# Optimization experiments

Hardware: AMD Instinct MI355X
Metric: run time of the kernel (lower is better)

Reference implementation:

```python
import jax, jax.numpy as jnp
import numpy as np

N = 100000
IN_C = 128
OUT_C = 32
HEADS = 4
E = 1600000
NEG_SLOPE = 0.2


def setup_inputs() -> dict:
    key = jax.random.key(0)
    ks = jax.random.split(key, 8)
    x = jax.random.normal(ks[0], (N, IN_C), dtype=jnp.float32)
    edge_index = jax.random.randint(ks[1], (2, E), 0, N, dtype=jnp.int64)
    # GATConv params (PyG conventions): lin weight [H*C, in], att vectors [H, C], bias [H*C]
    sc = 1.0 / np.sqrt(IN_C)
    W = jax.random.uniform(ks[2], (HEADS * OUT_C, IN_C), dtype=jnp.float32, minval=-sc, maxval=sc)
    att_src = jax.random.normal(ks[3], (HEADS, OUT_C), dtype=jnp.float32) * 0.1
    att_dst = jax.random.normal(ks[4], (HEADS, OUT_C), dtype=jnp.float32) * 0.1
    bias_conv = jnp.zeros((HEADS * OUT_C,), dtype=jnp.float32)
    # final nn.Linear(H*C, C)
    sl = 1.0 / np.sqrt(HEADS * OUT_C)
    W_lin = jax.random.uniform(ks[5], (OUT_C, HEADS * OUT_C), dtype=jnp.float32, minval=-sl, maxval=sl)
    b_lin = jax.random.uniform(ks[6], (OUT_C,), dtype=jnp.float32, minval=-sl, maxval=sl)
    return {"x": x, "edge_index": edge_index, "W": W, "att_src": att_src,
            "att_dst": att_dst, "bias_conv": bias_conv, "W_lin": W_lin, "b_lin": b_lin}


def reference(x, edge_index, W, att_src, att_dst, bias_conv, W_lin, b_lin):
    n = x.shape[0]
    # add self loops (PyG default)
    loops = jnp.arange(n, dtype=edge_index.dtype)
    src = jnp.concatenate([edge_index[0], loops])
    dst = jnp.concatenate([edge_index[1], loops])
    # linear projection, per-head split: [N, H, C]
    h = (x @ W.T).reshape(n, HEADS, OUT_C)
    # per-node attention logits
    a_src = jnp.einsum('nhc,hc->nh', h, att_src)  # [N, H]
    a_dst = jnp.einsum('nhc,hc->nh', h, att_dst)  # [N, H]
    e = a_src[src] + a_dst[dst]                   # [E', H]
    e = jax.nn.leaky_relu(e, NEG_SLOPE)
    # segment softmax over incoming edges per destination node
    m = jax.ops.segment_max(e, dst, num_segments=n)       # [N, H]
    e = jnp.exp(e - m[dst])
    s = jax.ops.segment_sum(e, dst, num_segments=n)       # [N, H]
    alpha = e / s[dst]                                    # [E', H]
    # scatter-aggregate alpha-weighted source features
    msg = alpha[:, :, None] * h[src]                      # [E', H, C]
    out = jax.ops.segment_sum(msg, dst, num_segments=n)   # [N, H, C]
    out = out.reshape(n, HEADS * OUT_C) + bias_conv
    # final linear + ELU
    return jax.nn.elu(out @ W_lin.T + b_lin)
```

## Files before the change

### kernel.cpp

```cpp
#include <hip/hip_runtime.h>
#include <hip/hip_fp16.h>
#include <cstdint>
#include <cstddef>

#define NHEADS 4
#define OUT_C 32
#define HC 128
#define IN_CH 128
#define NEG_SLOPE 0.2f
#define LDSPAD 136
#define KEDGE 4096

typedef _Float16 half8 __attribute__((ext_vector_type(8)));
typedef float floatx4 __attribute__((ext_vector_type(4)));

static inline size_t align256(size_t v) { return (v + 255) & ~(size_t)255; }

__device__ __forceinline__ float lrelu(float v) { return v > 0.f ? v : NEG_SLOPE * v; }

__device__ __forceinline__ float wred_sum(float v) {
    v += __shfl_xor(v, 1);
    v += __shfl_xor(v, 2);
    v += __shfl_xor(v, 4);
    v += __shfl_xor(v, 8);
    v += __shfl_xor(v, 16);
    v += __shfl_xor(v, 32);
    return v;
}

__device__ __forceinline__ unsigned int pack_h2(float a, float b) {
    __half2 h = __floats2half2_rn(a, b);
    return *reinterpret_cast<unsigned int*>(&h);
}
__device__ __forceinline__ float2 unpack_h2(unsigned int u) {
    __half2 h = *reinterpret_cast<__half2*>(&u);
    return __half22float2(h);
}

__device__ __forceinline__ int detect_f64(const int* __restrict__ ei, int E, int* sf) {
    int t = threadIdx.x;
    if (t == 0) *sf = 0;
    __syncthreads();
    int lim = E < 1024 ? E : 1024;
    int acc = 0;
    for (int i = t; i < lim; i += 256) acc |= ei[2 * i + 1];
    acc |= __shfl_xor(acc, 1);
    acc |= __shfl_xor(acc, 2);
    acc |= __shfl_xor(acc, 4);
    acc |= __shfl_xor(acc, 8);
    acc |= __shfl_xor(acc, 16);
    acc |= __shfl_xor(acc, 32);
    if ((t & 63) == 0 && acc) atomicOr(sf, 1);
    __syncthreads();
    return *sf == 0;
}

__global__ __launch_bounds__(256) void gemm_h(const float* __restrict__ x,
                                              const float* __restrict__ W,
                                              const float* __restrict__ att_src,
                                              const float* __restrict__ att_dst,
                                              __half* __restrict__ h,
                                              float* __restrict__ a_src,
                                              float* __restrict__ a_dst, int n) {
    __shared__ __align__(16) _Float16 Ws[128 * LDSPAD];
    __shared__ __align__(16) _Float16 Xs[128 * LDSPAD];
    int tid = threadIdx.x;
    int rowbase = blockIdx.x << 7;

    const float4* wf = (const float4*)W;
#pragma unroll
    for (int i = 0; i < 16; ++i) {
        int u = (i << 8) + tid;
        int r = u >> 5, g = u & 31;
        float4 v = wf[u];
        uint2 uu;
        uu.x = pack_h2(v.x, v.y);
        uu.y = pack_h2(v.z, v.w);
        *(uint2*)&Ws[r * LDSPAD + (g << 2)] = uu;
    }
    const float4* x4 = (const float4*)x;
#pragma unroll
    for (int i = 0; i < 16; ++i) {
        int u = (i << 8) + tid;
        int r = u >> 5, c4 = u & 31;
        int row = rowbase + r;
        if (row >= n) row = n - 1;
        float4 v = x4[((size_t)row << 5) + c4];
        uint2 uu;
        uu.x = pack_h2(v.x, v.y);
        uu.y = pack_h2(v.z, v.w);
        *(uint2*)&Xs[r * LDSPAD + (c4 << 2)] = uu;
    }
    __syncthreads();

    int lane = tid & 63, w = tid >> 6;
    int quad = lane >> 4, Lm = lane & 15;
    floatx4 acc[2][8];
#pragma unroll
    for (int rt = 0; rt < 2; ++rt)
#pragma unroll
        for (int c = 0; c < 8; ++c) acc[rt][c] = (floatx4){0.f, 0.f, 0.f, 0.f};

#pragma unroll
    for (int kc = 0; kc < 128; kc += 32) {
        int ko = kc + (quad << 3);
        half8 a0 = *(const half8*)&Xs[((w << 5) + Lm) * LDSPAD + ko];
        half8 a1 = *(const half8*)&Xs[((w << 5) + 16 + Lm) * LDSPAD + ko];
#pragma unroll
        for (int c = 0; c < 8; ++c) {
            half8 b = *(const half8*)&Ws[((c << 4) + Lm) * LDSPAD + ko];
            acc[0][c] = __builtin_amdgcn_mfma_f32_16x16x32_f16(a0, b, acc[0][c], 0, 0, 0);
            acc[1][c] = __builtin_amdgcn_mfma_f32_16x16x32_f16(a1, b, acc[1][c], 0, 0, 0);
        }
    }
    __syncthreads();
#pragma unroll
    for (int rt = 0; rt < 2; ++rt)
#pragma unroll
        for (int c = 0; c < 8; ++c)
#pragma unroll
            for (int i = 0; i < 4; ++i) {
                int rl = (w << 5) + (rt << 4) + (quad << 2) + i;
                int cl = (c << 4) + Lm;
                Xs[rl * LDSPAD + cl] = (_Float16)acc[rt][c][i];
            }
    __syncthreads();
#pragma unroll
    for (int i = 0; i < 8; ++i) {
        int u = (i << 8) + tid;
        int r = u >> 4, g = u & 15;
        int row = rowbase + r;
        if (row < n) {
            uint4 v = *(uint4*)&Xs[r * LDSPAD + (g << 3)];
            *(uint4*)(h + ((size_t)row << 7) + (g << 3)) = v;
        }
    }
    int r = tid >> 1, seg = tid & 1;
    int row = rowbase + r;
    const _Float16* hp = &Xs[r * LDSPAD + (seg << 6)];
    float sa = 0.f, da = 0.f, sb = 0.f, db = 0.f;
#pragma unroll
    for (int g8 = 0; g8 < 8; ++g8) {
        half8 v = *(const half8*)&hp[g8 << 3];
        int co = (seg << 6) + (g8 << 3);
        float4 A1 = *(const float4*)&att_src[co];
        float4 A2 = *(const float4*)&att_src[co + 4];
        float4 D1 = *(const float4*)&att_dst[co];
        float4 D2 = *(const float4*)&att_dst[co + 4];
        float f0 = (float)v[0], f1 = (float)v[1], f2 = (float)v[2], f3 = (float)v[3];
        float f4 = (float)v[4], f5 = (float)v[5], f6 = (float)v[6], f7 = (float)v[7];
        float ts = f0 * A1.x + f1 * A1.y + f2 * A1.z + f3 * A1.w
                 + f4 * A2.x + f5 * A2.y + f6 * A2.z + f7 * A2.w;
        float td = f0 * D1.x + f1 * D1.y + f2 * D1.z + f3 * D1.w
                 + f4 * D2.x + f5 * D2.y + f6 * D2.z + f7 * D2.w;
        if (g8 < 4) { sa += ts; da += td; } else { sb += ts; db += td; }
    }
    if (row < n) {
        int base = (row << 2) + (seg << 1);
        a_src[base] = sa;
        a_src[base + 1] = sb;
        a_dst[base] = da;
        a_dst[base + 1] = db;
    }
}

__global__ void bhist(const int* __restrict__ ei, int* __restrict__ bcount,
                      int E, int sh) {
    __shared__ int c[256];
    __shared__ int sf;
    int t = threadIdx.x;
    c[t] = 0;
    int f64 = detect_f64(ei, E, &sf);
    int stride = gridDim.x * 256;
    for (int i = blockIdx.x * 256 + t; i < E; i += stride) {
        int d;
        if (f64) d = (int)((const long long*)ei)[(size_t)E + i];
        else     d = ei[(size_t)E + i];
        atomicAdd(&c[d >> sh], 1);
    }
    __syncthreads();
    if (c[t]) atomicAdd(&bcount[t], c[t]);
}

__global__ __launch_bounds__(256) void bscatter(const int* __restrict__ ei,
                                                const int* __restrict__ bcount,
                                                int* __restrict__ gcursor,
                                                int2* __restrict__ bkt,
                                                int E, int n, int sh) {
    __shared__ int cnt[256], base[256], lcur[256], ts[256];
    __shared__ int sf;
    int t = threadIdx.x;
    cnt[t] = 0;
    lcur[t] = 0;
    int f64 = detect_f64(ei, E, &sf);
    int total = E + n;
    int i0 = blockIdx.x * KEDGE;
    int ed[16], es[16];
#pragma unroll
    for (int j = 0; j < 16; ++j) {
        int i = i0 + (j << 8) + t;
        int s = 0, d = -1;
        if (i < total) {
            if (i < E) {
                if (f64) {
                    s = (int)((const long long*)ei)[i];
                    d = (int)((const long long*)ei)[(size_t)E + i];
                } else {
                    s = ei[i];
                    d = ei[(size_t)E + i];
                }
            } else {
                s = d = i - E;
            }
            atomicAdd(&cnt[d >> sh], 1);
        }
        ed[j] = d;
        es[j] = s;
    }
    int lo = t << sh, hi = (t + 1) << sh;
    if (hi > n) hi = n;
    int nodes = hi > lo ? hi - lo : 0;
    int v = bcount[t] + nodes;
    ts[t] = v;
    __syncthreads();
    int run = v;
    for (int d = 1; d < 256; d <<= 1) {
        int o = (t >= d) ? ts[t - d] : 0;
        __syncthreads();
        run += o;
        ts[t] = run;
        __syncthreads();
    }
    int excl = run - v;
    base[t] = excl + (cnt[t] ? atomicAdd(&gcursor[t], cnt[t]) : 0);
    __syncthreads();
#pragma unroll
    for (int j = 0; j < 16; ++j) {
        int d = ed[j];
        if (d >= 0) {
            int b = d >> sh;
            int pos = base[b] + atomicAdd(&lcur[b], 1);
            bkt[pos] = make_int2(d, es[j]);
        }
    }
}

__global__ __launch_bounds__(256) void bsort(const int2* __restrict__ bkt,
                                             const int* __restrict__ bcount,
                                             int* __restrict__ off,
                                             int* __restrict__ sorted,
                                             int n, int E, int sh) {
    __shared__ int cnt[512], offl[512], ts[256];
    int t = threadIdx.x, bid = blockIdx.x;
    int lo = t << sh, hi = (t + 1) << sh;
    if (hi > n) hi = n;
    int nodes = hi > lo ? hi - lo : 0;
    int v = bcount[t] + nodes;
    ts[t] = v;
    __syncthreads();
    int run = v;
    for (int d = 1; d < 256; d <<= 1) {
        int o = (t >= d) ? ts[t - d] : 0;
        __syncthreads();
        run += o;
        ts[t] = run;
        __syncthreads();
    }
    int e0 = (bid > 0) ? ts[bid - 1] : 0;
    int e1 = ts[bid];
    if (bid == gridDim.x - 1 && t == 0) off[n] = E + n;
    int node0 = bid << sh;
    int node1 = (bid + 1) << sh;
    if (node1 > n) node1 = n;
    int nn = node1 - node0;
    __syncthreads();
    cnt[t] = 0;
    cnt[t + 256] = 0;
    __syncthreads();
    for (int i = e0 + t; i < e1; i += 256) {
        int2 e = bkt[i];
        atomicAdd(&cnt[e.x - node0], 1);
    }
    __syncthreads();
    int a = cnt[t << 1], b = cnt[(t << 1) + 1];
    int s = a + b;
    ts[t] = s;
    __syncthreads();
    run = s;
    for (int d = 1; d < 256; d <<= 1) {
        int o = (t >= d) ? ts[t - d] : 0;
        __syncthreads();
        run += o;
        ts[t] = run;
        __syncthreads();
    }
    int excl = run - s;
    offl[t << 1] = excl;
    offl[(t << 1) + 1] = excl + a;
    cnt[t << 1] = 0;
    cnt[(t << 1) + 1] = 0;
    __syncthreads();
    for (int i = t; i < nn; i += 256) off[node0 + i] = e0 + offl[i];
    for (int i = e0 + t; i < e1; i += 256) {
        int2 e = bkt[i];
        int li = e.x - node0;
        int pos = e0 + offl[li] + atomicAdd(&cnt[li], 1);
        sorted[pos] = e.y;
    }
}

__device__ __forceinline__ void accum_half(const int* ssrc, const float* sal,
                                           const __half* __restrict__ h,
                                           int deg, int half, int L, int head,
                                           float4& acc) {
    float4 a0 = {0, 0, 0, 0}, a1 = {0, 0, 0, 0}, a2 = {0, 0, 0, 0}, a3 = {0, 0, 0, 0};
    int j = half;
    for (; j + 14 < deg; j += 16) {
        int s0 = ssrc[j], s1 = ssrc[j + 2], s2 = ssrc[j + 4], s3 = ssrc[j + 6];
        int s4 = ssrc[j + 8], s5 = ssrc[j + 10], s6 = ssrc[j + 12], s7 = ssrc[j + 14];
        float w0 = sal[(j << 2) + head];
        float w1 = sal[((j + 2) << 2) + head];
        float w2 = sal[((j + 4) << 2) + head];
        float w3 = sal[((j + 6) << 2) + head];
        float w4 = sal[((j + 8) << 2) + head];
        float w5 = sal[((j + 10) << 2) + head];
        float w6 = sal[((j + 12) << 2) + head];
        float w7 = sal[((j + 14) << 2) + head];
        uint2 u0 = *(const uint2*)(h + ((size_t)s0 << 7) + (L << 2));
        uint2 u1 = *(const uint2*)(h + ((size_t)s1 << 7) + (L << 2));
        uint2 u2 = *(const uint2*)(h + ((size_t)s2 << 7) + (L << 2));
        uint2 u3 = *(const uint2*)(h + ((size_t)s3 << 7) + (L << 2));
        uint2 u4 = *(const uint2*)(h + ((size_t)s4 << 7) + (L << 2));
        uint2 u5 = *(const uint2*)(h + ((size_t)s5 << 7) + (L << 2));
        uint2 u6 = *(const uint2*)(h + ((size_t)s6 << 7) + (L << 2));
        uint2 u7 = *(const uint2*)(h + ((size_t)s7 << 7) + (L << 2));
        float2 fa, fb;
        fa = unpack_h2(u0.x); fb = unpack_h2(u0.y);
        a0.x = fmaf(w0, fa.x, a0.x); a0.y = fmaf(w0, fa.y, a0.y);
        a0.z = fmaf(w0, fb.x, a0.z); a0.w = fmaf(w0, fb.y, a0.w);
        fa = unpack_h2(u1.x); fb = unpack_h2(u1.y);
        a1.x = fmaf(w1, fa.x, a1.x); a1.y = fmaf(w1, fa.y, a1.y);
        a1.z = fmaf(w1, fb.x, a1.z); a1.w = fmaf(w1, fb.y, a1.w);
        fa = unpack_h2(u2.x); fb = unpack_h2(u2.y);
        a2.x = fmaf(w2, fa.x, a2.x); a2.y = fmaf(w2, fa.y, a2.y);
        a2.z = fmaf(w2, fb.x, a2.z); a2.w = fmaf(w2, fb.y, a2.w);
        fa = unpack_h2(u3.x); fb = unpack_h2(u3.y);
        a3.x = fmaf(w3, fa.x, a3.x); a3.y = fmaf(w3, fa.y, a3.y);
        a3.z = fmaf(w3, fb.x, a3.z); a3.w = fmaf(w3, fb.y, a3.w);
        fa = unpack_h2(u4.x); fb = unpack_h2(u4.y);
        a0.x = fmaf(w4, fa.x, a0.x); a0.y = fmaf(w4, fa.y, a0.y);
        a0.z = fmaf(w4, fb.x, a0.z); a0.w = fmaf(w4, fb.y, a0.w);
        fa = unpack_h2(u5.x); fb = unpack_h2(u5.y);
        a1.x = fmaf(w5, fa.x, a1.x); a1.y = fmaf(w5, fa.y, a1.y);
        a1.z = fmaf(w5, fb.x, a1.z); a1.w = fmaf(w5, fb.y, a1.w);
        fa = unpack_h2(u6.x); fb = unpack_h2(u6.y);
        a2.x = fmaf(w6, fa.x, a2.x); a2.y = fmaf(w6, fa.y, a2.y);
        a2.z = fmaf(w6, fb.x, a2.z); a2.w = fmaf(w6, fb.y, a2.w);
        fa = unpack_h2(u7.x); fb = unpack_h2(u7.y);
        a3.x = fmaf(w7, fa.x, a3.x); a3.y = fmaf(w7, fa.y, a3.y);
        a3.z = fmaf(w7, fb.x, a3.z); a3.w = fmaf(w7, fb.y, a3.w);
    }
    for (; j + 6 < deg; j += 8) {
        int s0 = ssrc[j], s1 = ssrc[j + 2], s2 = ssrc[j + 4], s3 = ssrc[j + 6];
        float w0 = sal[(j << 2) + head];
        float w1 = sal[((j + 2) << 2) + head];
        float w2 = sal[((j + 4) << 2) + head];
        float w3 = sal[((j + 6) << 2) + head];
        uint2 u0 = *(const uint2*)(h + ((size_t)s0 << 7) + (L << 2));
        uint2 u1 = *(const uint2*)(h + ((size_t)s1 << 7) + (L << 2));
        uint2 u2 = *(const uint2*)(h + ((size_t)s2 << 7) + (L << 2));
        uint2 u3 = *(const uint2*)(h + ((size_t)s3 << 7) + (L << 2));
        float2 fa, fb;
        fa = unpack_h2(u0.x); fb = unpack_h2(u0.y);
        a0.x = fmaf(w0, fa.x, a0.x); a0.y = fmaf(w0, fa.y, a0.y);
        a0.z = fmaf(w0, fb.x, a0.z); a0.w = fmaf(w0, fb.y, a0.w);
        fa = unpack_h2(u1.x); fb = unpack_h2(u1.y);
        a1.x = fmaf(w1, fa.x, a1.x); a1.y = fmaf(w1, fa.y, a1.y);
        a1.z = fmaf(w1, fb.x, a1.z); a1.w = fmaf(w1, fb.y, a1.w);
        fa = unpack_h2(u2.x); fb = unpack_h2(u2.y);
        a2.x = fmaf(w2, fa.x, a2.x); a2.y = fmaf(w2, fa.y, a2.y);
        a2.z = fmaf(w2, fb.x, a2.z); a2.w = fmaf(w2, fb.y, a2.w);
        fa = unpack_h2(u3.x); fb = unpack_h2(u3.y);
        a3.x = fmaf(w3, fa.x, a3.x); a3.y = fmaf(w3, fa.y, a3.y);
        a3.z = fmaf(w3, fb.x, a3.z); a3.w = fmaf(w3, fb.y, a3.w);
    }
    for (; j < deg; j += 2) {
        int s0 = ssrc[j];
        float w0 = sal[(j << 2) + head];
        uint2 u0 = *(const uint2*)(h + ((size_t)s0 << 7) + (L << 2));
        float2 fa = unpack_h2(u0.x), fb = unpack_h2(u0.y);
        a0.x = fmaf(w0, fa.x, a0.x); a0.y = fmaf(w0, fa.y, a0.y);
        a0.z = fmaf(w0, fb.x, a0.z); a0.w = fmaf(w0, fb.y, a0.w);
    }
    acc.x += (a0.x + a1.x) + (a2.x + a3.x);
    acc.y += (a0.y + a1.y) + (a2.y + a3.y);
    acc.z += (a0.z + a1.z) + (a2.z + a3.z);
    acc.w += (a0.w + a1.w) + (a2.w + a3.w);
}

__global__ __launch_bounds__(256) void aggregate(const __half* __restrict__ h,
                                                 const int* __restrict__ sorted,
                                                 const int* __restrict__ off,
                                                 const float* __restrict__ a_src,
                                                 const float* __restrict__ a_dst,
                                                 const float* __restrict__ bias,
                                                 __half* __restrict__ agg, int n) {
    __shared__ __align__(16) int sh_src[4][64];
    __shared__ __align__(16) float sh_al[4][256];
    int wslot = threadIdx.x >> 6;
    int lane = threadIdx.x & 63;
    int wid = blockIdx.x * 4 + wslot;
    int nw = gridDim.x * 4;
    int L = lane & 31, half = lane >> 5, head = L >> 3;
    float4 b4 = ((const float4*)bias)[L];
    const float4* as4 = (const float4*)a_src;
    const float4* ad4 = (const float4*)a_dst;
    int* ssrc = sh_src[wslot];
    float* sal = sh_al[wslot];

    for (int node = wid; node < n; node += nw) {
        int start = off[node], end = off[node + 1];
        int deg = end - start;
        float4 ad = ad4[node];
        float4 acc = {0.f, 0.f, 0.f, 0.f};
        float4 psum = {0.f, 0.f, 0.f, 0.f};

        if (deg <= 64) {
            bool v = lane < deg;
            int idx = start + (v ? lane : 0);
            int s = sorted[idx];
            float4 as = as4[s];
            float4 p;
            p.x = v ? __expf(lrelu(as.x + ad.x)) : 0.f;
            p.y = v ? __expf(lrelu(as.y + ad.y)) : 0.f;
            p.z = v ? __expf(lrelu(as.z + ad.z)) : 0.f;
            p.w = v ? __expf(lrelu(as.w + ad.w)) : 0.f;
            psum = p;
            ssrc[lane] = s;
            *(float4*)&sal[lane << 2] = p;
            asm volatile("s_waitcnt lgkmcnt(0)" ::: "memory");
            accum_half(ssrc, sal, h, deg, half, L, head, acc);
            asm volatile("" ::: "memory");
        } else {
            for (int bb = 0; bb < deg; bb += 64) {
                int i = bb + lane;
                bool v = i < deg;
                int idx = start + (v ? i : 0);
                int s = sorted[idx];
                float4 as = as4[s];
                float4 p;
                p.x = v ? __expf(lrelu(as.x + ad.x)) : 0.f;
                p.y = v ? __expf(lrelu(as.y + ad.y)) : 0.f;
                p.z = v ? __expf(lrelu(as.z + ad.z)) : 0.f;
                p.w = v ? __expf(lrelu(as.w + ad.w)) : 0.f;
                psum.x += p.x; psum.y += p.y; psum.z += p.z; psum.w += p.w;
                ssrc[lane] = s;
                *(float4*)&sal[lane << 2] = p;
                asm volatile("s_waitcnt lgkmcnt(0)" ::: "memory");
                int cl = deg - bb;
                if (cl > 64) cl = 64;
                accum_half(ssrc, sal, h, cl, half, L, head, acc);
                asm volatile("" ::: "memory");
            }
        }
        float s0 = wred_sum(psum.x), s1 = wred_sum(psum.y);
        float s2 = wred_sum(psum.z), s3 = wred_sum(psum.w);
        float sh = (head == 0) ? s0 : (head == 1) ? s1 : (head == 2) ? s2 : s3;
        float inv = 1.f / sh;
        acc.x += __shfl_xor(acc.x, 32);
        acc.y += __shfl_xor(acc.y, 32);
        acc.z += __shfl_xor(acc.z, 32);
        acc.w += __shfl_xor(acc.w, 32);
        if (lane < 32) {
            float4 res = {fmaf(acc.x, inv, b4.x), fmaf(acc.y, inv, b4.y),
                          fmaf(acc.z, inv, b4.z), fmaf(acc.w, inv, b4.w)};
            uint2 u;
            u.x = pack_h2(res.x, res.y);
            u.y = pack_h2(res.z, res.w);
            *(uint2*)(agg + ((size_t)node << 7) + (L << 2)) = u;
        }
    }
}

__global__ __launch_bounds__(256) void proj(const __half* __restrict__ agg,
                                            const float* __restrict__ W_lin,
                                            const float* __restrict__ b_lin,
                                            float* __restrict__ out, int n) {
    __shared__ float xs[64][132];
    __shared__ float wt[128][36];
    int tid = threadIdx.x;
    const float4* w4 = (const float4*)W_lin;
#pragma unroll
    for (int i = 0; i < 4; ++i) {
        int f4 = (i << 8) + tid;
        int o = f4 >> 5, kk = (f4 & 31) << 2;
        float4 w = w4[f4];
        wt[kk][o] = w.x;
        wt[kk + 1][o] = w.y;
        wt[kk + 2][o] = w.z;
        wt[kk + 3][o] = w.w;
    }
    int rowbase = blockIdx.x << 6;
    const uint4* a4 = (const uint4*)agg;
#pragma unroll
    for (int i = 0; i < 4; ++i) {
        int f8 = (i << 8) + tid;
        int r = f8 >> 4, cc = (f8 & 15) << 3;
        int row = rowbase + r;
        if (row >= n) row = n - 1;
        uint4 u = a4[((size_t)row << 4) + (cc >> 3)];
        float2 f0 = unpack_h2(u.x), f1 = unpack_h2(u.y);
        float2 f2 = unpack_h2(u.z), f3 = unpack_h2(u.w);
        float* xp = &xs[r][cc];
        xp[0] = f0.x; xp[1] = f0.y; xp[2] = f1.x; xp[3] = f1.y;
        xp[4] = f2.x; xp[5] = f2.y; xp[6] = f3.x; xp[7] = f3.y;
    }
    __syncthreads();
    int r = tid >> 2, cg = tid & 3, c0 = cg << 3;
    float acc[8];
#pragma unroll
    for (int j = 0; j < 8; ++j) acc[j] = 0.f;
    for (int k = 0; k < 128; k += 4) {
        float4 xv = *(const float4*)&xs[r][k];
        float xk[4] = {xv.x, xv.y, xv.z, xv.w};
#pragma unroll
        for (int kk = 0; kk < 4; ++kk) {
            float4 wa = *(const float4*)&wt[k + kk][c0];
            float4 wb = *(const float4*)&wt[k + kk][c0 + 4];
            acc[0] = fmaf(xk[kk], wa.x, acc[0]);
            acc[1] = fmaf(xk[kk], wa.y, acc[1]);
            acc[2] = fmaf(xk[kk], wa.z, acc[2]);
            acc[3] = fmaf(xk[kk], wa.w, acc[3]);
            acc[4] = fmaf(xk[kk], wb.x, acc[4]);
            acc[5] = fmaf(xk[kk], wb.y, acc[5]);
            acc[6] = fmaf(xk[kk], wb.z, acc[6]);
            acc[7] = fmaf(xk[kk], wb.w, acc[7]);
        }
    }
    int row = rowbase + r;
    if (row < n) {
        float res[8];
#pragma unroll
        for (int j = 0; j < 8; ++j) {
            float v = acc[j] + b_lin[c0 + j];
            res[j] = v > 0.f ? v : (__expf(v) - 1.f);
        }
        float4* op = (float4*)(out + (size_t)row * 32 + c0);
        op[0] = make_float4(res[0], res[1], res[2], res[3]);
        op[1] = make_float4(res[4], res[5], res[6], res[7]);
    }
}

extern "C" void kernel_launch(void* const* d_in, const int* in_sizes, int n_in,
                              void* d_out, int out_size, void* d_ws, size_t ws_size,
                              hipStream_t stream) {
    const float* x = (const float*)d_in[0];
    const int* ei = (const int*)d_in[1];
    const float* W = (const float*)d_in[2];
    const float* att_src = (const float*)d_in[3];
    const float* att_dst = (const float*)d_in[4];
    const float* bias_conv = (const float*)d_in[5];
    const float* W_lin = (const float*)d_in[6];
    const float* b_lin = (const float*)d_in[7];
    int n = in_sizes[0] / IN_CH;
    int E = in_sizes[1] / 2;

    int sh = 0;
    while (((n + (1 << sh) - 1) >> sh) > 256) sh++;
    int NB = (n + (1 << sh) - 1) >> sh;

    char* ws = (char*)d_ws;
    size_t o = 0;
    auto alloc = [&](size_t bytes) { char* p = ws + o; o = align256(o + bytes); return p; };
    __half* h      = (__half*)alloc((size_t)n * HC * 2);
    __half* agg    = (__half*)alloc((size_t)n * HC * 2);
    float* a_src   = (float*)alloc((size_t)n * NHEADS * 4);
    float* a_dst   = (float*)alloc((size_t)n * NHEADS * 4);
    int* off       = (int*)alloc(((size_t)n + 1) * 4);
    int* bcount    = (int*)alloc(256 * 4);
    int* gcursor   = (int*)alloc(256 * 4);
    int* sorted    = (int*)alloc((size_t)(E + n + 64) * 4);
    int2* bkt      = (int2*)alloc((size_t)(E + n + 64) * 8);

    hipMemsetAsync(bcount, 0, 2048, stream);

    gemm_h<<<(n + 127) / 128, 256, 0, stream>>>(x, W, att_src, att_dst, h, a_src, a_dst, n);
    bhist<<<1024, 256, 0, stream>>>(ei, bcount, E, sh);
    bscatter<<<(E + n + KEDGE - 1) / KEDGE, 256, 0, stream>>>(ei, bcount, gcursor, bkt, E, n, sh);
    bsort<<<NB, 256, 0, stream>>>(bkt, bcount, off, sorted, n, E, sh);
    aggregate<<<2048, 256, 0, stream>>>(h, sorted, off, a_src, a_dst, bias_conv, agg, n);
    proj<<<(n + 63) / 64, 256, 0, stream>>>(agg, W_lin, b_lin, (float*)d_out, n);
}
```

Before: 303.3 us.

## Fuse histogram into GEMM launch and final projection into aggregation

The bucket histogram now runs as extra blocks in the same launch as the projection GEMM, so the two independent stages execute concurrently and one launch is removed. The final linear layer plus ELU is folded into the aggregation kernel: each wave writes its 128-wide aggregated row to LDS and computes the 32 outputs from an LDS copy of W_lin. This drops the fp16 agg intermediate round trip through global memory and the separate proj launch. In exchange the aggregate kernel uses more LDS (about 17KB for W_lin) and does per-node projection work, and the GEMM kernel's 68KB LDS footprint now also applies to the histogram blocks.

New measurement: 414.9 us. 1.37x slower.

```diff
diff --git a/kernel.cpp b/kernel.cpp
--- a/kernel.cpp
+++ b/kernel.cpp
@@ -10,6 +10,7 @@
 #define NEG_SLOPE 0.2f
 #define LDSPAD 136
 #define KEDGE 4096
+#define WLP 133
 
 typedef _Float16 half8 __attribute__((ext_vector_type(8)));
 typedef float floatx4 __attribute__((ext_vector_type(4)));
@@ -55,16 +56,37 @@
     return *sf == 0;
 }
 
-__global__ __launch_bounds__(256) void gemm_h(const float* __restrict__ x,
-                                              const float* __restrict__ W,
-                                              const float* __restrict__ att_src,
-                                              const float* __restrict__ att_dst,
-                                              __half* __restrict__ h,
-                                              float* __restrict__ a_src,
-                                              float* __restrict__ a_dst, int n) {
+__global__ __launch_bounds__(256) void gemm_hist(const float* __restrict__ x,
+                                                 const float* __restrict__ W,
+                                                 const float* __restrict__ att_src,
+                                                 const float* __restrict__ att_dst,
+                                                 __half* __restrict__ h,
+                                                 float* __restrict__ a_src,
+                                                 float* __restrict__ a_dst, int n,
+                                                 const int* __restrict__ ei,
+                                                 int* __restrict__ bcount,
+                                                 int E, int sh, int GB) {
     __shared__ __align__(16) _Float16 Ws[128 * LDSPAD];
     __shared__ __align__(16) _Float16 Xs[128 * LDSPAD];
+    __shared__ int hc[256];
+    __shared__ int sf;
     int tid = threadIdx.x;
+
+    if (blockIdx.x >= GB) {
+        hc[tid] = 0;
+        int f64 = detect_f64(ei, E, &sf);
+        int nbh = gridDim.x - GB;
+        int stride = nbh * 256;
+        for (int i = (blockIdx.x - GB) * 256 + tid; i < E; i += stride) {
+            int d;
+            if (f64) d = (int)((const long long*)ei)[(size_t)E + i];
+            else     d = ei[(size_t)E + i];
+            atomicAdd(&hc[d >> sh], 1);
+        }
+        __syncthreads();
+        if (hc[tid]) atomicAdd(&bcount[tid], hc[tid]);
+        return;
+    }
     int rowbase = blockIdx.x << 7;
 
     const float4* wf = (const float4*)W;
@@ -162,24 +184,6 @@
         a_dst[base] = da;
         a_dst[base + 1] = db;
     }
-}
-
-__global__ void bhist(const int* __restrict__ ei, int* __restrict__ bcount,
-                      int E, int sh) {
-    __shared__ int c[256];
-    __shared__ int sf;
-    int t = threadIdx.x;
-    c[t] = 0;
-    int f64 = detect_f64(ei, E, &sf);
-    int stride = gridDim.x * 256;
-    for (int i = blockIdx.x * 256 + t; i < E; i += stride) {
-        int d;
-        if (f64) d = (int)((const long long*)ei)[(size_t)E + i];
-        else     d = ei[(size_t)E + i];
-        atomicAdd(&c[d >> sh], 1);
-    }
-    __syncthreads();
-    if (c[t]) atomicAdd(&bcount[t], c[t]);
 }
 
 __global__ __launch_bounds__(256) void bscatter(const int* __restrict__ ei,
@@ -404,11 +408,24 @@
                                                  const float* __restrict__ a_src,
                                                  const float* __restrict__ a_dst,
                                                  const float* __restrict__ bias,
-                                                 __half* __restrict__ agg, int n) {
+                                                 const float* __restrict__ W_lin,
+                                                 const float* __restrict__ b_lin,
+                                                 float* __restrict__ out, int n) {
     __shared__ __align__(16) int sh_src[4][64];
     __shared__ __align__(16) float sh_al[4][256];
-    int wslot = threadIdx.x >> 6;
-    int lane = threadIdx.x & 63;
+    __shared__ __align__(16) float sh_res[4][128];
+    __shared__ __align__(16) float Wl[32 * WLP];
+    __shared__ float sbl[32];
+    int tid = threadIdx.x;
+    for (int i = tid; i < 4096; i += 256) {
+        int o = i >> 7, k = i & 127;
+        Wl[o * WLP + k] = W_lin[i];
+    }
+    if (tid < 32) sbl[tid] = b_lin[tid];
+    __syncthreads();
+
+    int wslot = tid >> 6;
+    int lane = tid & 63;
     int wid = blockIdx.x * 4 + wslot;
     int nw = gridDim.x * 4;
     int L = lane & 31, half = lane >> 5, head = L >> 3;
@@ -417,6 +434,9 @@
     const float4* ad4 = (const float4*)a_dst;
     int* ssrc = sh_src[wslot];
     float* sal = sh_al[wslot];
+    float* sres = sh_res[wslot];
+    const float* wrow = &Wl[L * WLP + (half << 6)];
+    const float* rrow = &sres[half << 6];
 
     for (int node = wid; node < n; node += nw) {
         int start = off[node], end = off[node + 1];
@@ -474,80 +494,31 @@
         if (lane < 32) {
             float4 res = {fmaf(acc.x, inv, b4.x), fmaf(acc.y, inv, b4.y),
                           fmaf(acc.z, inv, b4.z), fmaf(acc.w, inv, b4.w)};
-            uint2 u;
-            u.x = pack_h2(res.x, res.y);
-            u.y = pack_h2(res.z, res.w);
-            *(uint2*)(agg + ((size_t)node << 7) + (L << 2)) = u;
-        }
-    }
-}
-
-__global__ __launch_bounds__(256) void proj(const __half* __restrict__ agg,
-                                            const float* __restrict__ W_lin,
-                                            const float* __restrict__ b_lin,
-                                            float* __restrict__ out, int n) {
-    __shared__ float xs[64][132];
-    __shared__ float wt[128][36];
-    int tid = threadIdx.x;
-    const float4* w4 = (const float4*)W_lin;
-#pragma unroll
-    for (int i = 0; i < 4; ++i) {
-        int f4 = (i << 8) + tid;
-        int o = f4 >> 5, kk = (f4 & 31) << 2;
-        float4 w = w4[f4];
-        wt[kk][o] = w.x;
-        wt[kk + 1][o] = w.y;
-        wt[kk + 2][o] = w.z;
-        wt[kk + 3][o] = w.w;
-    }
-    int rowbase = blockIdx.x << 6;
-    const uint4* a4 = (const uint4*)agg;
-#pragma unroll
-    for (int i = 0; i < 4; ++i) {
-        int f8 = (i << 8) + tid;
-        int r = f8 >> 4, cc = (f8 & 15) << 3;
-        int row = rowbase + r;
-        if (row >= n) row = n - 1;
-        uint4 u = a4[((size_t)row << 4) + (cc >> 3)];
-        float2 f0 = unpack_h2(u.x), f1 = unpack_h2(u.y);
-        float2 f2 = unpack_h2(u.z), f3 = unpack_h2(u.w);
-        float* xp = &xs[r][cc];
-        xp[0] = f0.x; xp[1] = f0.y; xp[2] = f1.x; xp[3] = f1.y;
-        xp[4] = f2.x; xp[5] = f2.y; xp[6] = f3.x; xp[7] = f3.y;
-    }
-    __syncthreads();
-    int r = tid >> 2, cg = tid & 3, c0 = cg << 3;
-    float acc[8];
-#pragma unroll
-    for (int j = 0; j < 8; ++j) acc[j] = 0.f;
-    for (int k = 0; k < 128; k += 4) {
-        float4 xv = *(const float4*)&xs[r][k];
-        float xk[4] = {xv.x, xv.y, xv.z, xv.w};
-#pragma unroll
-        for (int kk = 0; kk < 4; ++kk) {
-            float4 wa = *(const float4*)&wt[k + kk][c0];
-            float4 wb = *(const float4*)&wt[k + kk][c0 + 4];
-            acc[0] = fmaf(xk[kk], wa.x, acc[0]);
-            acc[1] = fmaf(xk[kk], wa.y, acc[1]);
-            acc[2] = fmaf(xk[kk], wa.z, acc[2]);
-            acc[3] = fmaf(xk[kk], wa.w, acc[3]);
-            acc[4] = fmaf(xk[kk], wb.x, acc[4]);
-            acc[5] = fmaf(xk[kk], wb.y, acc[5]);
-            acc[6] = fmaf(xk[kk], wb.z, acc[6]);
-            acc[7] = fmaf(xk[kk], wb.w, acc[7]);
-        }
-    }
-    int row = rowbase + r;
-    if (row < n) {
-        float res[8];
-#pragma unroll
-        for (int j = 0; j < 8; ++j) {
-            float v = acc[j] + b_lin[c0 + j];
-            res[j] = v > 0.f ? v : (__expf(v) - 1.f);
-        }
-        float4* op = (float4*)(out + (size_t)row * 32 + c0);
-        op[0] = make_float4(res[0], res[1], res[2], res[3]);
-        op[1] = make_float4(res[4], res[5], res[6], res[7]);
+            *(float4*)&sres[L << 2] = res;
+        }
+        asm volatile("s_waitcnt lgkmcnt(0)" ::: "memory");
+        float sum = 0.f;
+#pragma unroll
+        for (int k4 = 0; k4 < 64; k4 += 8) {
+            float4 r1 = *(const float4*)&rrow[k4];
+            float4 r2 = *(const float4*)&rrow[k4 + 4];
+            float4 w1 = *(const float4*)&wrow[k4];
+            float4 w2 = *(const float4*)&wrow[k4 + 4];
+            sum = fmaf(r1.x, w1.x, sum);
+            sum = fmaf(r1.y, w1.y, sum);
+            sum = fmaf(r1.z, w1.z, sum);
+            sum = fmaf(r1.w, w1.w, sum);
+            sum = fmaf(r2.x, w2.x, sum);
+            sum = fmaf(r2.y, w2.y, sum);
+            sum = fmaf(r2.z, w2.z, sum);
+            sum = fmaf(r2.w, w2.w, sum);
+        }
+        sum += __shfl_xor(sum, 32);
+        if (lane < 32) {
+            float v = sum + sbl[L];
+            out[(size_t)node * 32 + L] = v > 0.f ? v : __expf(v) - 1.f;
+        }
+        asm volatile("" ::: "memory");
     }
 }
 
@@ -573,7 +544,6 @@
     size_t o = 0;
     auto alloc = [&](size_t bytes) { char* p = ws + o; o = align256(o + bytes); return p; };
     __half* h      = (__half*)alloc((size_t)n * HC * 2);
-    __half* agg    = (__half*)alloc((size_t)n * HC * 2);
     float* a_src   = (float*)alloc((size_t)n * NHEADS * 4);
     float* a_dst   = (float*)alloc((size_t)n * NHEADS * 4);
     int* off       = (int*)alloc(((size_t)n + 1) * 4);
@@ -584,10 +554,12 @@
 
     hipMemsetAsync(bcount, 0, 2048, stream);
 
-    gemm_h<<<(n + 127) / 128, 256, 0, stream>>>(x, W, att_src, att_dst, h, a_src, a_dst, n);
-    bhist<<<1024, 256, 0, stream>>>(ei, bcount, E, sh);
+    int GB = (n + 127) / 128;
+    int NBH = 1024;
+    gemm_hist<<<GB + NBH, 256, 0, stream>>>(x, W, att_src, att_dst, h, a_src, a_dst, n,
+                                            ei, bcount, E, sh, GB);
     bscatter<<<(E + n + KEDGE - 1) / KEDGE, 256, 0, stream>>>(ei, bcount, gcursor, bkt, E, n, sh);
     bsort<<<NB, 256, 0, stream>>>(bkt, bcount, off, sorted, n, E, sh);
-    aggregate<<<2048, 256, 0, stream>>>(h, sorted, off, a_src, a_dst, bias_conv, agg, n);
-    proj<<<(n + 63) / 64, 256, 0, stream>>>(agg, W_lin, b_lin, (float*)d_out, n);
-}
+    aggregate<<<2048, 256, 0, stream>>>(h, sorted, off, a_src, a_dst, bias_conv,
+                                        W_lin, b_lin, (float*)d_out, n);
+}
```
